# Kernel optimization log

Hardware: AMD Instinct MI355X
Metric: run time of the kernel (lower is better)

The kernel has to match this reference:

```python
import jax, jax.numpy as jnp
import numpy as np

B, N, D, H, F = 2, 2048, 512, 8, 8
HD = D // H

def setup_inputs() -> dict:
    key = jax.random.key(0)
    ks = jax.random.split(key, 11)
    s = 1.0 / np.sqrt(D)
    return {
        "x": jax.random.normal(ks[0], (B, N, D), dtype=jnp.float32),
        "phase_coords": jax.random.uniform(ks[1], (B, N, F), dtype=jnp.float32) * 6.28,
        "Wq": jax.random.normal(ks[2], (D, D), dtype=jnp.float32) * s,
        "bq": jax.random.normal(ks[3], (D,), dtype=jnp.float32) * 0.01,
        "Wk": jax.random.normal(ks[4], (D, D), dtype=jnp.float32) * s,
        "bk": jax.random.normal(ks[5], (D,), dtype=jnp.float32) * 0.01,
        "Wv": jax.random.normal(ks[6], (D, D), dtype=jnp.float32) * s,
        "bv": jax.random.normal(ks[7], (D,), dtype=jnp.float32) * 0.01,
        "Wo": jax.random.normal(ks[8], (D, D), dtype=jnp.float32) * s,
        "bo": jax.random.normal(ks[9], (D,), dtype=jnp.float32) * 0.01,
        "phase_bias": jax.random.normal(ks[10], (H, F), dtype=jnp.float32) * 0.1,
    }

def reference(x, phase_coords, Wq, bq, Wk, bk, Wv, bv, Wo, bo, phase_bias):
    b, n, _ = x.shape
    def proj(W, bias):
        # [B,N,D] -> [B,H,N,HD]
        return (x @ W.T + bias).reshape(b, n, H, HD).transpose(0, 2, 1, 3)
    Q, K, V = proj(Wq, bq), proj(Wk, bk), proj(Wv, bv)
    scores = jnp.einsum("bhqd,bhkd->bhqk", Q, K) / np.sqrt(HD)
    # phase coherence bias: cos of pairwise phase diffs, weighted per head
    phase_diff = phase_coords[:, :, None, :] - phase_coords[:, None, :, :]  # [B,N,N,F]
    coherence = jnp.cos(phase_diff)
    bias = jnp.einsum("bqkf,hf->bhqk", coherence, phase_bias)
    scores = scores + bias
    attn = jax.nn.softmax(scores, axis=-1)
    attended = jnp.einsum("bhqk,bhkd->bhqd", attn, V)
    attended = attended.transpose(0, 2, 1, 3).reshape(b, n, D)
    return attended @ Wo.T + bo
```

## Files before the change

kernel.cpp:

```cpp
#include <hip/hip_runtime.h>
#include <stdint.h>

typedef unsigned short u16;
typedef unsigned int   u32;
typedef __bf16 bf16x8 __attribute__((ext_vector_type(8)));
typedef float  f32x4  __attribute__((ext_vector_type(4)));
typedef u16    u16x8  __attribute__((ext_vector_type(8)));
typedef u16    u16x4  __attribute__((ext_vector_type(4)));

#define B_  2
#define N_  2048
#define D_  512
#define H_  8
#define HD_ 64
#define QKD 96
#define LOG2E 1.4426950408889634f

__device__ __forceinline__ u16 f2bf(float f) {
  union { float f; u32 u; } v; v.f = f;
  u32 r = v.u + 0x7FFFu + ((v.u >> 16) & 1u);
  return (u16)(r >> 16);
}
__device__ __forceinline__ u16 f2bf_trunc(float f) {
  union { float f; u32 u; } v; v.f = f;
  return (u16)(v.u >> 16);
}
__device__ __forceinline__ void gload_lds16(const void* g, void* l) {
  __builtin_amdgcn_global_load_lds(
      (const __attribute__((address_space(1))) void*)g,
      (__attribute__((address_space(3))) void*)l, 16, 0, 0);
}

__global__ __launch_bounds__(256) void k_prep(
    const float* __restrict__ x, const float* __restrict__ pc,
    const float* __restrict__ Wq, const float* __restrict__ bq,
    const float* __restrict__ Wk, const float* __restrict__ bk,
    const float* __restrict__ Wv, const float* __restrict__ bv,
    const float* __restrict__ Wo, const float* __restrict__ pb,
    u16* __restrict__ xb, u16* __restrict__ wqkvb, float* __restrict__ bqkv,
    u16* __restrict__ wob, u16* __restrict__ Qe, u16* __restrict__ Ke)
{
  int gid = blockIdx.x * blockDim.x + threadIdx.x;
  int stride = gridDim.x * blockDim.x;
  const float qs = 0.125f * LOG2E;
  for (int i = gid; i < B_ * N_ * D_; i += stride) xb[i] = f2bf(x[i]);
  for (int i = gid; i < 3 * D_ * D_; i += stride) {
    int r = i >> 9;
    float v;
    if (r < 512)       v = Wq[i] * qs;
    else if (r < 1024) v = Wk[i - 512 * 512];
    else               v = Wv[i - 1024 * 512];
    wqkvb[i] = f2bf(v);
  }
  for (int i = gid; i < 3 * D_; i += stride) {
    float v;
    if (i < 512)       v = bq[i] * qs;
    else if (i < 1024) v = bk[i - 512];
    else               v = bv[i - 1024];
    bqkv[i] = v;
  }
  for (int i = gid; i < D_ * D_; i += stride) wob[i] = f2bf(Wo[i]);

  for (int i = gid; i < 16 * N_; i += stride) {
    int bh = i >> 11, n = i & 2047;
    int b = bh >> 3, h = bh & 7;
    u16x8 qc, qsn, kc, ksn, z;
#pragma unroll
    for (int f = 0; f < 8; f++) {
      float a = pc[((size_t)b * N_ + n) * 8 + f];
      float cv = __cosf(a), sv = __sinf(a);
      float w = pb[h * 8 + f] * LOG2E;
      qc[f]  = f2bf(w * cv);  qsn[f] = f2bf(w * sv);
      kc[f]  = f2bf(cv);      ksn[f] = f2bf(sv);
      z[f] = 0;
    }
    size_t base = ((size_t)bh * N_ + n) * QKD;
    *(u16x8*)&Qe[base + 64] = qc;  *(u16x8*)&Qe[base + 72] = qsn;
    *(u16x8*)&Qe[base + 80] = z;   *(u16x8*)&Qe[base + 88] = z;
    *(u16x8*)&Ke[base + 64] = kc;  *(u16x8*)&Ke[base + 72] = ksn;
    *(u16x8*)&Ke[base + 80] = z;   *(u16x8*)&Ke[base + 88] = z;
  }
}

template <int MODE, int BN>
__global__ __launch_bounds__(256) void k_gemm(
    const u16* __restrict__ A, const u16* __restrict__ Bm,
    const float* __restrict__ bias,
    u16* __restrict__ Qe, u16* __restrict__ Ke, u16* __restrict__ Vt,
    float* __restrict__ Of)
{
  constexpr int JT  = BN / 32;
  constexpr int BNC = BN / 32;
  __shared__ u16 As[3][64 * 64];
  __shared__ u16 Bs[3][BN * 64];
  const int tid = threadIdx.x;
  const int wave = tid >> 6, lane = tid & 63;
  const int fr = lane & 15, kg = lane >> 4;
  const int m0 = blockIdx.x * 64, n0 = blockIdx.y * BN;
  const int wr = (wave >> 1) * 32, wc = (wave & 1) * (BN / 2);

  f32x4 acc[2][JT];
#pragma unroll
  for (int i = 0; i < 2; i++)
#pragma unroll
    for (int j = 0; j < JT; j++)
#pragma unroll
      for (int r = 0; r < 4; r++) acc[i][j][r] = 0.f;

  auto stage = [&](int buf, int k0) {
#pragma unroll
    for (int u = 0; u < 2; u++) {
      int chunk = (wave * 2 + u) * 64 + lane;
      int row = chunk >> 3, cl = chunk & 7;
      gload_lds16(A + (size_t)(m0 + row) * 512 + k0 + ((cl ^ (row & 7)) << 3),
                  &As[buf][(wave * 2 + u) * 512]);
    }
#pragma unroll
    for (int u = 0; u < BNC; u++) {
      int chunk = (wave * BNC + u) * 64 + lane;
      int row = chunk >> 3, cl = chunk & 7;
      gload_lds16(Bm + (size_t)(n0 + row) * 512 + k0 + ((cl ^ (row & 7)) << 3),
                  &Bs[buf][(wave * BNC + u) * 512]);
    }
  };

  stage(0, 0);
  stage(1, 64);

#pragma unroll
  for (int s = 0; s < 8; s++) {
    if (s < 7) {
      if constexpr (BN == 128) asm volatile("s_waitcnt vmcnt(6)" ::: "memory");
      else                     asm volatile("s_waitcnt vmcnt(4)" ::: "memory");
    } else {
      asm volatile("s_waitcnt vmcnt(0)" ::: "memory");
    }
    asm volatile("s_waitcnt lgkmcnt(0)" ::: "memory");
    __builtin_amdgcn_sched_barrier(0);
    __builtin_amdgcn_s_barrier();
    __builtin_amdgcn_sched_barrier(0);
    if (s < 6) stage((s + 2) % 3, (s + 2) * 64);
    const int cb = s % 3;
#pragma unroll
    for (int ksub = 0; ksub < 2; ksub++) {
      bf16x8 af[2], bf[JT];
#pragma unroll
      for (int i = 0; i < 2; i++)
        af[i] = *(const bf16x8*)&As[cb][(wr + i * 16 + fr) * 64 + (((ksub * 4 + kg) ^ (fr & 7)) << 3)];
#pragma unroll
      for (int j = 0; j < JT; j++)
        bf[j] = *(const bf16x8*)&Bs[cb][(wc + j * 16 + fr) * 64 + (((ksub * 4 + kg) ^ (fr & 7)) << 3)];
#pragma unroll
      for (int i = 0; i < 2; i++)
#pragma unroll
        for (int j = 0; j < JT; j++)
          acc[i][j] = __builtin_amdgcn_mfma_f32_16x16x32_bf16(af[i], bf[j], acc[i][j], 0, 0, 0);
    }
  }

  if (MODE == 1) {
#pragma unroll
    for (int j = 0; j < JT; j++) {
      int col = n0 + wc + j * 16 + fr;
      float bc = bias[col];
#pragma unroll
      for (int i = 0; i < 2; i++)
#pragma unroll
        for (int r = 0; r < 4; r++)
          Of[(size_t)(m0 + wr + i * 16 + kg * 4 + r) * 512 + col] = acc[i][j][r] + bc;
  } } else {
    const int seg = n0 >> 9;
    const int nb = n0 & 511;
    if (seg < 2) {
      u16* dst = seg ? Ke : Qe;
#pragma unroll
      for (int j = 0; j < JT; j++) {
        int col = nb + wc + j * 16 + fr;
        float bc = bias[n0 + wc + j * 16 + fr];
        int h = col >> 6, d = col & 63;
#pragma unroll
        for (int i = 0; i < 2; i++) {
#pragma unroll
          for (int r = 0; r < 4; r++) {
            int row = m0 + wr + i * 16 + kg * 4 + r;
            int b = row >> 11, nn = row & 2047;
            dst[((size_t)(b * 8 + h) * N_ + nn) * QKD + d] = f2bf(acc[i][j][r] + bc);
          }
        }
      }
    } else {
#pragma unroll
      for (int j = 0; j < JT; j++) {
        int cc = nb + wc + j * 16 + fr;
        float bc = bias[n0 + wc + j * 16 + fr];
        int h = cc >> 6, d = cc & 63;
#pragma unroll
        for (int i = 0; i < 2; i++) {
          int row = m0 + wr + i * 16 + kg * 4;
          int b = row >> 11, n = row & 2047;
          u16x4 o;
#pragma unroll
          for (int r = 0; r < 4; r++) o[r] = f2bf(acc[i][j][r] + bc);
          *(u16x4*)&Vt[((size_t)(b * 8 + h) * 64 + d) * N_ + n] = o;
        }
      }
    }
  }
}

__global__ __launch_bounds__(256, 3) void k_attn(
    const u16* __restrict__ Qe, const u16* __restrict__ Ke,
    const u16* __restrict__ Vt, u16* __restrict__ attb)
{
  const int bh = blockIdx.x, b = bh >> 3, h = bh & 7;
  const int q0 = blockIdx.y * 128;
  const int tid = threadIdx.x, wave = tid >> 6, lane = tid & 63;
  const int fr = lane & 15, kg = lane >> 4;

  __shared__ u16 Klds[2][64 * 96];
  __shared__ u16 Vlds[64 * 64];
  __shared__ u16 Plds[4][32 * 64];

  auto stageK = [&](int buf, int kv) {
#pragma unroll
    for (int p = 0; p < 3; p++) {
      u32 c = p * 256 + tid;
      u32 r = c / 12u, s = c - r * 12u;
      u32 g = (s < 8) ? (s ^ (r & 7)) : (8 + ((s & 3) ^ (r & 3)));
      gload_lds16(Ke + ((size_t)bh * N_ + kv + r) * QKD + g * 8,
                  &Klds[buf][(p * 256 + wave * 64) * 8]);
    }
  };
  auto stageV = [&](int kv) {
#pragma unroll
    for (int p = 0; p < 2; p++) {
      int c = p * 256 + tid;
      int row = c >> 3, c8 = c & 7;
      gload_lds16(Vt + ((size_t)bh * 64 + row) * N_ + kv + ((c8 ^ (row & 7)) << 3),
                  &Vlds[(p * 256 + wave * 64) * 8]);
    }
  };

  bf16x8 qa[2][3];
#pragma unroll
  for (int i = 0; i < 2; i++) {
    size_t gq = (size_t)bh * N_ + q0 + wave * 32 + i * 16 + fr;
#pragma unroll
    for (int ks = 0; ks < 3; ks++)
      qa[i][ks] = *(const bf16x8*)&Qe[gq * QKD + ks * 32 + kg * 8];
  }

  f32x4 accO[2][4];
#pragma unroll
  for (int i = 0; i < 2; i++)
#pragma unroll
    for (int d = 0; d < 4; d++)
#pragma unroll
      for (int r = 0; r < 4; r++) accO[i][d][r] = 0.f;
  float Lacc[2][4];
#pragma unroll
  for (int i = 0; i < 2; i++)
#pragma unroll
    for (int r = 0; r < 4; r++) Lacc[i][r] = 0.f;

  stageK(0, 0);
  stageV(0);
  stageK(1, 64);

  for (int t = 0; t < 32; t++) {
    const int cb = t & 1;
    if (t < 31) asm volatile("s_waitcnt vmcnt(3)" ::: "memory");
    else        asm volatile("s_waitcnt vmcnt(0)" ::: "memory");
    __builtin_amdgcn_sched_barrier(0);
    __builtin_amdgcn_s_barrier();
    __builtin_amdgcn_sched_barrier(0);

    f32x4 accS[2][4];
#pragma unroll
    for (int i = 0; i < 2; i++)
#pragma unroll
      for (int j = 0; j < 4; j++)
#pragma unroll
        for (int r = 0; r < 4; r++) accS[i][j][r] = 0.f;

    __builtin_amdgcn_s_setprio(1);
#pragma unroll
    for (int ks = 0; ks < 3; ks++) {
#pragma unroll
      for (int j = 0; j < 4; j++) {
        int slot = (ks < 2) ? ((ks * 4 + kg) ^ (fr & 7)) : (8 + (kg ^ (fr & 3)));
        bf16x8 kb = *(const bf16x8*)&Klds[cb][(j * 16 + fr) * 96 + slot * 8];
#pragma unroll
        for (int i = 0; i < 2; i++)
          accS[i][j] = __builtin_amdgcn_mfma_f32_16x16x32_bf16(qa[i][ks], kb, accS[i][j], 0, 0, 0);
      }
    }
    __builtin_amdgcn_s_setprio(0);

#pragma unroll
    for (int i = 0; i < 2; i++) {
#pragma unroll
      for (int j = 0; j < 4; j++) {
#pragma unroll
        for (int r = 0; r < 4; r++) {
          float p = __builtin_amdgcn_exp2f(accS[i][j][r] - 11.5415603f);
          Lacc[i][r] += p;
          int rw = i * 16 + kg * 4 + r;
          Plds[wave][rw * 64 + ((j * 16 + fr) ^ ((rw & 7) << 3))] = f2bf_trunc(p);
        }
      }
    }
    asm volatile("s_waitcnt lgkmcnt(0)" ::: "memory");
    __builtin_amdgcn_sched_barrier(0);

    __builtin_amdgcn_s_setprio(1);
#pragma unroll
    for (int ks = 0; ks < 2; ks++) {
      bf16x8 pa[2];
#pragma unroll
      for (int i = 0; i < 2; i++)
        pa[i] = *(const bf16x8*)&Plds[wave][(i * 16 + fr) * 64 + ((ks * 32 + kg * 8) ^ ((fr & 7) << 3))];
#pragma unroll
      for (int d = 0; d < 4; d++) {
        bf16x8 vb = *(const bf16x8*)&Vlds[(d * 16 + fr) * 64 + (((ks * 4 + kg) ^ (fr & 7)) << 3)];
#pragma unroll
        for (int i = 0; i < 2; i++)
          accO[i][d] = __builtin_amdgcn_mfma_f32_16x16x32_bf16(pa[i], vb, accO[i][d], 0, 0, 0);
      }
    }
    __builtin_amdgcn_s_setprio(0);

    __builtin_amdgcn_sched_barrier(0);
    __builtin_amdgcn_s_barrier();
    __builtin_amdgcn_sched_barrier(0);
    if (t + 1 < 32) stageV((t + 1) * 64);
    if (t + 2 < 32) stageK(cb, (t + 2) * 64);
  }

#pragma unroll
  for (int i = 0; i < 2; i++) {
#pragma unroll
    for (int r = 0; r < 4; r++) {
      float l = Lacc[i][r];
      l += __shfl_xor(l, 1); l += __shfl_xor(l, 2);
      l += __shfl_xor(l, 4); l += __shfl_xor(l, 8);
      float inv = 1.0f / l;
      int qg = q0 + wave * 32 + i * 16 + kg * 4 + r;
#pragma unroll
      for (int d = 0; d < 4; d++)
        attb[(size_t)(b * N_ + qg) * 512 + h * 64 + d * 16 + fr] = f2bf(accO[i][d][r] * inv);
    }
  }
}

extern "C" void kernel_launch(void* const* d_in, const int* in_sizes, int n_in,
                              void* d_out, int out_size, void* d_ws, size_t ws_size,
                              hipStream_t stream)
{
  (void)in_sizes; (void)n_in; (void)out_size; (void)ws_size;
  const float* x  = (const float*)d_in[0];
  const float* pc = (const float*)d_in[1];
  const float* Wq = (const float*)d_in[2];
  const float* bq = (const float*)d_in[3];
  const float* Wk = (const float*)d_in[4];
  const float* bk = (const float*)d_in[5];
  const float* Wv = (const float*)d_in[6];
  const float* bv = (const float*)d_in[7];
  const float* Wo = (const float*)d_in[8];
  const float* bo = (const float*)d_in[9];
  const float* pb = (const float*)d_in[10];

  u16* ws = (u16*)d_ws;
  const size_t TOK = (size_t)B_ * N_;
  u16* xb    = ws;
  u16* Qe    = xb    + TOK * D_;
  u16* Ke    = Qe    + (size_t)16 * N_ * QKD;
  u16* Vt    = Ke    + (size_t)16 * N_ * QKD;
  u16* attb  = Vt    + TOK * D_;
  u16* wqkvb = attb  + TOK * D_;
  u16* wob   = wqkvb + (size_t)3 * D_ * D_;
  float* bqkv = (float*)(wob + (size_t)D_ * D_);

  k_prep<<<1024, 256, 0, stream>>>(x, pc, Wq, bq, Wk, bk, Wv, bv, Wo, pb,
                                   xb, wqkvb, bqkv, wob, Qe, Ke);
  k_gemm<0, 128><<<dim3(64, 12), 256, 0, stream>>>(xb, wqkvb, bqkv, Qe, Ke, Vt, nullptr);
  k_attn<<<dim3(16, 16), 256, 0, stream>>>(Qe, Ke, Vt, attb);
  k_gemm<1, 64><<<dim3(64, 8), 256, 0, stream>>>(attb, wob, bo, nullptr, nullptr, nullptr, (float*)d_out);
}
```

Baseline: 158.4 us.

## Double-buffer V tiles in attention and split phase-feature prep across threads

New measurement: 158.9 us. About the same (+0.3%).

```diff
diff --git a/kernel.cpp b/kernel.cpp
--- a/kernel.cpp
+++ b/kernel.cpp
@@ -61,24 +61,26 @@
   }
   for (int i = gid; i < D_ * D_; i += stride) wob[i] = f2bf(Wo[i]);
 
-  for (int i = gid; i < 16 * N_; i += stride) {
-    int bh = i >> 11, n = i & 2047;
+  for (int i = gid; i < 16 * N_ * 4; i += stride) {
+    int idx = i >> 2, part = i & 3;
+    int bh = idx >> 11, n = idx & 2047;
     int b = bh >> 3, h = bh & 7;
-    u16x8 qc, qsn, kc, ksn, z;
-#pragma unroll
-    for (int f = 0; f < 8; f++) {
-      float a = pc[((size_t)b * N_ + n) * 8 + f];
-      float cv = __cosf(a), sv = __sinf(a);
-      float w = pb[h * 8 + f] * LOG2E;
-      qc[f]  = f2bf(w * cv);  qsn[f] = f2bf(w * sv);
-      kc[f]  = f2bf(cv);      ksn[f] = f2bf(sv);
-      z[f] = 0;
-    }
-    size_t base = ((size_t)bh * N_ + n) * QKD;
-    *(u16x8*)&Qe[base + 64] = qc;  *(u16x8*)&Qe[base + 72] = qsn;
-    *(u16x8*)&Qe[base + 80] = z;   *(u16x8*)&Qe[base + 88] = z;
-    *(u16x8*)&Ke[base + 64] = kc;  *(u16x8*)&Ke[base + 72] = ksn;
-    *(u16x8*)&Ke[base + 80] = z;   *(u16x8*)&Ke[base + 88] = z;
+    size_t base = ((size_t)bh * N_ + n) * QKD + 64 + part * 8;
+    u16x8 qv, kv;
+    if (part < 2) {
+#pragma unroll
+      for (int f = 0; f < 8; f++) {
+        float a = pc[((size_t)b * N_ + n) * 8 + f];
+        float t = (part == 0) ? __cosf(a) : __sinf(a);
+        kv[f] = f2bf(t);
+        qv[f] = f2bf(pb[h * 8 + f] * LOG2E * t);
+      }
+    } else {
+#pragma unroll
+      for (int f = 0; f < 8; f++) { qv[f] = 0; kv[f] = 0; }
+    }
+    *(u16x8*)&Qe[base] = qv;
+    *(u16x8*)&Ke[base] = kv;
   }
 }
 
@@ -218,7 +220,7 @@
   const int fr = lane & 15, kg = lane >> 4;
 
   __shared__ u16 Klds[2][64 * 96];
-  __shared__ u16 Vlds[64 * 64];
+  __shared__ u16 Vlds[2][64 * 64];
   __shared__ u16 Plds[4][32 * 64];
 
   auto stageK = [&](int buf, int kv) {
@@ -231,13 +233,13 @@
                   &Klds[buf][(p * 256 + wave * 64) * 8]);
     }
   };
-  auto stageV = [&](int kv) {
+  auto stageV = [&](int buf, int kv) {
 #pragma unroll
     for (int p = 0; p < 2; p++) {
       int c = p * 256 + tid;
       int row = c >> 3, c8 = c & 7;
       gload_lds16(Vt + ((size_t)bh * 64 + row) * N_ + kv + ((c8 ^ (row & 7)) << 3),
-                  &Vlds[(p * 256 + wave * 64) * 8]);
+                  &Vlds[buf][(p * 256 + wave * 64) * 8]);
     }
   };
 
@@ -264,12 +266,13 @@
     for (int r = 0; r < 4; r++) Lacc[i][r] = 0.f;
 
   stageK(0, 0);
-  stageV(0);
+  stageV(0, 0);
   stageK(1, 64);
+  stageV(1, 64);
 
   for (int t = 0; t < 32; t++) {
     const int cb = t & 1;
-    if (t < 31) asm volatile("s_waitcnt vmcnt(3)" ::: "memory");
+    if (t < 31) asm volatile("s_waitcnt vmcnt(5)" ::: "memory");
     else        asm volatile("s_waitcnt vmcnt(0)" ::: "memory");
     __builtin_amdgcn_sched_barrier(0);
     __builtin_amdgcn_s_barrier();
@@ -322,7 +325,7 @@
         pa[i] = *(const bf16x8*)&Plds[wave][(i * 16 + fr) * 64 + ((ks * 32 + kg * 8) ^ ((fr & 7) << 3))];
 #pragma unroll
       for (int d = 0; d < 4; d++) {
-        bf16x8 vb = *(const bf16x8*)&Vlds[(d * 16 + fr) * 64 + (((ks * 4 + kg) ^ (fr & 7)) << 3)];
+        bf16x8 vb = *(const bf16x8*)&Vlds[cb][(d * 16 + fr) * 64 + (((ks * 4 + kg) ^ (fr & 7)) << 3)];
 #pragma unroll
         for (int i = 0; i < 2; i++)
           accO[i][d] = __builtin_amdgcn_mfma_f32_16x16x32_bf16(pa[i], vb, accO[i][d], 0, 0, 0);
@@ -333,8 +336,10 @@
     __builtin_amdgcn_sched_barrier(0);
     __builtin_amdgcn_s_barrier();
     __builtin_amdgcn_sched_barrier(0);
-    if (t + 1 < 32) stageV((t + 1) * 64);
-    if (t + 2 < 32) stageK(cb, (t + 2) * 64);
+    if (t + 2 < 32) {
+      stageV(cb, (t + 2) * 64);
+      stageK(cb, (t + 2) * 64);
+    }
   }
 
 #pragma unroll
```
